# Kernel tuning notes

Measured on AMD Instinct MI355X. Metric: run time of the kernel, lower is better.

Reference implementation:

```python
import jax, jax.numpy as jnp
import numpy as np

B, S, NC, ND, V = 16, 512, 10000, 10000, 128


def _rn(k, shape, scale=0.05):
    return jax.random.normal(k, shape, dtype=jnp.float32) * scale


def setup_inputs() -> dict:
    key = jax.random.key(0)
    ks = jax.random.split(key, 24)
    inp = {
        'c_seq': jax.random.randint(ks[0], (B, S), 0, NC),
        'd_seq': jax.random.randint(ks[1], (B, S), 0, ND),
        'r_seq': jax.random.uniform(ks[2], (B, S), dtype=jnp.float32),
        # embeddings / vectors
        'D1_w': _rn(ks[3], (ND, 1)),
        'D2_w': _rn(ks[4], (ND, V)),
        'v_r': _rn(ks[5], (V,)),
        'v_beta': _rn(ks[6], (V,)),
        # GRU (torch layout: gates ordered r,z,n; W_ih [3V,2V], W_hh [3V,V])
        'W_ih': _rn(ks[7], (3 * V, 2 * V)),
        'W_hh': _rn(ks[8], (3 * V, V)),
        'b_ih': jnp.zeros((3 * V,), jnp.float32),
        'b_hh': jnp.zeros((3 * V,), jnp.float32),
        # linear_1: V -> V -> V -> 1 (weights stored [in, out])
        'm1_W1': _rn(ks[9], (V, V)), 'm1_b1': jnp.zeros((V,), jnp.float32),
        'm1_W2': _rn(ks[10], (V, V)), 'm1_b2': jnp.zeros((V,), jnp.float32),
        'm1_W3': _rn(ks[11], (V, 1)), 'm1_b3': jnp.zeros((1,), jnp.float32),
        # linear_2: 3V -> V -> V -> 1
        'm2_W1': _rn(ks[12], (3 * V, V)), 'm2_b1': jnp.zeros((V,), jnp.float32),
        'm2_W2': _rn(ks[13], (V, V)), 'm2_b2': jnp.zeros((V,), jnp.float32),
        'm2_W3': _rn(ks[14], (V, 1)), 'm2_b3': jnp.zeros((1,), jnp.float32),
    }
    return inp


def _mlp(x, W1, b1, W2, b2, W3, b3):
    h = jax.nn.relu(x @ W1 + b1)
    h = jax.nn.relu(h @ W2 + b2)
    return h @ W3 + b3


def _gru_seq(x, W_ih, W_hh, b_ih, b_hh):
    # x: [B,S,2V] -> h_seq [B,S,V]; torch GRU gate order r,z,n
    xp = x @ W_ih.T + b_ih  # [B,S,3V]

    def step(h, xt):
        hp = h @ W_hh.T + b_hh
        xr, xz, xn = jnp.split(xt, 3, axis=-1)
        hr, hz, hn = jnp.split(hp, 3, axis=-1)
        r = jax.nn.sigmoid(xr + hr)
        z = jax.nn.sigmoid(xz + hz)
        n = jnp.tanh(xn + r * hn)
        h_new = (1.0 - z) * n + z * h
        return h_new, h_new

    h0 = jnp.zeros((x.shape[0], W_hh.shape[1]), x.dtype)
    _, hs = jax.lax.scan(step, h0, jnp.swapaxes(xp, 0, 1))  # [S,B,V]
    return jnp.swapaxes(hs, 0, 1)


def reference(c_seq, d_seq, r_seq, D1_w, D2_w, v_r, v_beta,
              W_ih, W_hh, b_ih, b_hh,
              m1_W1, m1_b1, m1_W2, m1_b2, m1_W3, m1_b3,
              m2_W1, m2_b1, m2_W2, m2_b2, m2_W3, m2_b3):
    v_d_seq = D2_w[d_seq]                     # [B,S,V]
    v_r_seq = r_seq[..., None] * v_r          # [B,S,V]

    h_seq = _gru_seq(jnp.concatenate([v_d_seq, v_r_seq], axis=-1),
                     W_ih, W_hh, b_ih, b_hh)  # [B,S,V]
    alpha_seq = _mlp(h_seq, m1_W1, m1_b1, m1_W2, m1_b2, m1_W3, m1_b3)[..., 0]  # [B,S]

    bidx = jnp.arange(c_seq.shape[0])

    def step(C, ins):
        c_t, vd_t, vr_t = ins                 # [B], [B,V], [B,V]
        beta_prev = C[bidx, c_t]              # gather: [B]
        v_beta_prev = beta_prev[:, None] * v_beta  # [B,V]
        new_c = _mlp(jnp.concatenate([v_beta_prev, vd_t, vr_t], axis=-1),
                     m2_W1, m2_b1, m2_W2, m2_b2, m2_W3, m2_b3)[:, 0]  # [B]
        C = C.at[bidx, c_t].set(new_c)        # scatter
        return C, (C, new_c)

    C0 = jnp.zeros((c_seq.shape[0], NC), jnp.float32)
    _, (C_seq, beta_seq) = jax.lax.scan(
        step, C0,
        (jnp.swapaxes(c_seq, 0, 1), jnp.swapaxes(v_d_seq, 0, 1), jnp.swapaxes(v_r_seq, 0, 1)))
    C_seq = jnp.swapaxes(C_seq, 0, 1)[..., None]   # [B,S,NC,1]
    beta_seq = jnp.swapaxes(beta_seq, 0, 1)        # [B,S]

    gamma_seq = D1_w[d_seq][..., 0]                # [B,S]
    return (alpha_seq, beta_seq, gamma_seq, h_seq, C_seq)
```

## Files before the change

### kernel.cpp

```cpp
#include <hip/hip_runtime.h>

#define Bq   16
#define Sq   512
#define Vq   128
#define NCq  10000

#define OFF_XP     0u
#define OFF_PRE1   3145728u
#define OFF_WTIH   4194304u
#define OFF_W2T    4243456u
#define OFF_WVRIH  4292608u
#define OFF_WVR1   4292992u
#define OFF_WVB    4293120u
#define OFF_PO     4293248u

__global__ __launch_bounds__(256) void k0_prep(
    const int* __restrict__ c_seq, const int* __restrict__ d_seq,
    const float* __restrict__ D1_w,
    const float* __restrict__ W_ih,
    const float* __restrict__ v_r, const float* __restrict__ v_beta,
    const float* __restrict__ m2W1, const float* __restrict__ m2W2,
    float* __restrict__ ws, float* __restrict__ gamma_out)
{
    const int blk = blockIdx.x, tid = threadIdx.x;

    if (blk < 128) {
        float* WTIH = ws + OFF_WTIH;
        int base = blk * 384;
        for (int i = tid; i < 384; i += 256) {
            int e = base + i;
            int k = e / 384, g = e % 384;
            WTIH[e] = W_ih[g * 256 + k];
        }
    } else if (blk == 128) {
        float* WVRIH = ws + OFF_WVRIH;
        float* WVR1  = ws + OFF_WVR1;
        float* WVB   = ws + OFF_WVB;
        for (int g = tid; g < 384; g += 256) {
            float a = 0.f;
            for (int k = 0; k < 128; ++k) a = fmaf(v_r[k], W_ih[g * 256 + 128 + k], a);
            WVRIH[g] = a;
        }
        if (tid < 128) {
            float a = 0.f, b = 0.f;
            for (int k = 0; k < 128; ++k) {
                a = fmaf(v_r[k],    m2W1[(256 + k) * 128 + tid], a);
                b = fmaf(v_beta[k], m2W1[k * 128 + tid],         b);
            }
            WVR1[tid] = a; WVB[tid] = b;
        }
    } else if (blk < 145) {
        const int b = blk - 129;
        __shared__ int cs[Sq];
        for (int i = tid; i < Sq; i += 256) cs[i] = c_seq[b * Sq + i];
        __syncthreads();
        int* PO = (int*)(ws + OFF_PO) + b * Sq;
        for (int t = tid; t < Sq; t += 256) {
            int c = cs[t];
            int po = -1;
            for (int u = t - 1; u >= 0; --u) if (cs[u] == c) { po = u; break; }
            PO[t] = po;
        }
    } else if (blk < 161) {
        const int b = blk - 145;
        for (int s = tid; s < Sq; s += 256)
            gamma_out[b * Sq + s] = D1_w[d_seq[b * Sq + s]];
    } else {
        float* W2T = ws + OFF_W2T;
        for (int e = tid; e < 16384; e += 256) {
            int j = e >> 7, k = e & 127;
            W2T[e] = m2W2[k * 128 + j];
        }
    }
}

__global__ __launch_bounds__(256) void k1_gemm(
    const int* __restrict__ d_seq, const float* __restrict__ D2_w,
    const float* __restrict__ m2W1, float* __restrict__ ws)
{
    __shared__ float As[64 * 128];
    __shared__ float Bs[128 * 64];
    const int blk = blockIdx.x, tid = threadIdx.x;
    const int nc = blk & 7;
    const int m0 = (blk >> 3) * 64;
    const float* WTIH = ws + OFF_WTIH;

    const float4* D2v = (const float4*)D2_w;
    for (int e = tid; e < 2048; e += 256) {
        int r = e >> 5, q = e & 31;
        int d = d_seq[m0 + r];
        *(float4*)&As[r * 128 + 4 * q] = D2v[d * 32 + q];
    }
    for (int e = tid; e < 2048; e += 256) {
        int k = e >> 4, q = e & 15;
        float4 v;
        if (nc < 6) v = *(const float4*)&WTIH[k * 384 + nc * 64 + 4 * q];
        else        v = *(const float4*)&m2W1[(128 + k) * 128 + (nc - 6) * 64 + 4 * q];
        *(float4*)&Bs[k * 64 + 4 * q] = v;
    }
    __syncthreads();

    const int tx = tid & 15, ty = tid >> 4;
    const int c0 = 4 * tx, r0 = 4 * ty;
    float acc[4][4];
#pragma unroll
    for (int i = 0; i < 4; ++i)
#pragma unroll
        for (int j = 0; j < 4; ++j) acc[i][j] = 0.f;

    for (int k = 0; k < 128; ++k) {
        float4 bv = *(const float4*)&Bs[k * 64 + c0];
#pragma unroll
        for (int i = 0; i < 4; ++i) {
            float a = As[(r0 + i) * 128 + k];
            acc[i][0] = fmaf(a, bv.x, acc[i][0]);
            acc[i][1] = fmaf(a, bv.y, acc[i][1]);
            acc[i][2] = fmaf(a, bv.z, acc[i][2]);
            acc[i][3] = fmaf(a, bv.w, acc[i][3]);
        }
    }
    float* XP   = ws + OFF_XP;
    float* PRE1 = ws + OFF_PRE1;
#pragma unroll
    for (int i = 0; i < 4; ++i) {
        int row = m0 + r0 + i;
        float4 v = make_float4(acc[i][0], acc[i][1], acc[i][2], acc[i][3]);
        if (nc < 6) *(float4*)&XP[row * 384 + nc * 64 + c0] = v;
        else        *(float4*)&PRE1[row * 128 + (nc - 6) * 64 + c0] = v;
    }
}

__global__ __launch_bounds__(384, 1) void k2_scan(
    const float* __restrict__ r_seq, const float* __restrict__ W_hh,
    const float* __restrict__ b_ih, const float* __restrict__ b_hh,
    const float* __restrict__ m2b1, const float* __restrict__ m2b2,
    const float* __restrict__ m2W3, const float* __restrict__ m2b3,
    float* __restrict__ ws,
    float* __restrict__ hseq_out, float* __restrict__ beta_out)
{
    __shared__ union {
        struct { float h[128]; float sumr[128]; float sumz[128]; float r[512]; } g;
        struct { float bh[512]; float h1[128]; float red[2]; float r2[512]; int po_[512]; } bt;
    } sm;

    const int blk = blockIdx.x, tid = threadIdx.x;
    const int j = tid & 127;

    if (blk < 16) {
        const int b = blk;
        const int role = tid >> 7;
        const int grow = (role == 0) ? 256 + j : ((role == 1) ? j : 128 + j);

        float4 w4[32];
        {
            const float4* wr = (const float4*)(W_hh + grow * 128);
#pragma unroll
            for (int kk = 0; kk < 32; ++kk) w4[kk] = wr[kk];
        }
        const float wvr = (ws + OFF_WVRIH)[grow];
        const float bih = b_ih[grow];
        const float bhh = b_hh[grow];
        for (int i = tid; i < Sq; i += 384) sm.g.r[i] = r_seq[b * Sq + i];
        if (tid < 128) sm.g.h[tid] = 0.f;
        float h_old = 0.f;
        __syncthreads();

        const float* xpb = ws + OFF_XP + (size_t)b * Sq * 384;
        float xp0 = xpb[grow];
        float xp1 = xpb[384 + grow];
        const float4* h4 = (const float4*)sm.g.h;

        for (int t = 0; t < Sq; ++t) {
            float xp2 = (t < Sq - 2) ? xpb[(t + 2) * 384 + grow] : 0.f;
            float x = fmaf(sm.g.r[t], wvr, xp0 + bih);
            float a0 = 0.f, a1 = 0.f, a2 = 0.f, a3 = 0.f;
#pragma unroll
            for (int kk = 0; kk < 32; ++kk) {
                float4 hv = h4[kk];
                float4 wv = w4[kk];
                a0 = fmaf(wv.x, hv.x, a0);
                a1 = fmaf(wv.y, hv.y, a1);
                a2 = fmaf(wv.z, hv.z, a2);
                a3 = fmaf(wv.w, hv.w, a3);
            }
            float hp = (a0 + a1) + (a2 + a3) + bhh;
            if (role == 1) sm.g.sumr[j] = x + hp;
            else if (role == 2) sm.g.sumz[j] = x + hp;
            __syncthreads();
            if (role == 0) {
                float r = 1.f / (1.f + __expf(-sm.g.sumr[j]));
                float z = 1.f / (1.f + __expf(-sm.g.sumz[j]));
                float npre = fmaf(r, hp, x);
                float ax = fabsf(npre);
                float e2 = __expf(-2.f * ax);
                float n = copysignf((1.f - e2) / (1.f + e2), npre);
                float hnew = (1.f - z) * n + z * h_old;
                h_old = hnew;
                sm.g.h[j] = hnew;
                hseq_out[(size_t)(b * Sq + t) * 128 + j] = hnew;
            }
            __syncthreads();
            xp0 = xp1; xp1 = xp2;
        }
    } else {
        const int b = blk - 16;
        float4 w24[32];
        {
            const float4* wr = (const float4*)(ws + OFF_W2T + j * 128);
#pragma unroll
            for (int kk = 0; kk < 32; ++kk) w24[kk] = wr[kk];
        }
        float wvbj = 0.f, wvr1j = 0.f, b1j = 0.f, b2j = 0.f, w3j = 0.f;
        if (tid < 128) {
            wvbj  = (ws + OFF_WVB)[j];
            wvr1j = (ws + OFF_WVR1)[j];
            b1j = m2b1[j]; b2j = m2b2[j]; w3j = m2W3[j];
        }
        const float b3v = m2b3[0];
        const int* PO = (const int*)(ws + OFF_PO) + b * Sq;
        for (int i = tid; i < Sq; i += 384) {
            sm.bt.r2[i]  = r_seq[b * Sq + i];
            sm.bt.po_[i] = PO[i];
        }
        __syncthreads();

        const float* p1b = ws + OFF_PRE1 + (size_t)b * Sq * 128;
        float p1 = (tid < 128) ? p1b[j] : 0.f;
        const float4* h14 = (const float4*)sm.bt.h1;
        float btap = 0.f;

        for (int t = 0; t < Sq; ++t) {
            float p1n = (tid < 128 && t < Sq - 1) ? p1b[(t + 1) * 128 + j] : 0.f;
            if (tid < 128) {
                int po = sm.bt.po_[t];
                float bp = (po == t - 1) ? btap : ((po >= 0) ? sm.bt.bh[po] : 0.f);
                sm.bt.h1[j] = fmaxf(0.f, fmaf(bp, wvbj, fmaf(sm.bt.r2[t], wvr1j, p1 + b1j)));
            } else if (tid == 128 && t > 0) {
                sm.bt.bh[t - 1] = btap;
            }
            __syncthreads();
            if (tid < 128) {
                float a0 = 0.f, a1 = 0.f, a2 = 0.f, a3 = 0.f;
#pragma unroll
                for (int kk = 0; kk < 32; ++kk) {
                    float4 hv = h14[kk];
                    float4 wv = w24[kk];
                    a0 = fmaf(wv.x, hv.x, a0);
                    a1 = fmaf(wv.y, hv.y, a1);
                    a2 = fmaf(wv.z, hv.z, a2);
                    a3 = fmaf(wv.w, hv.w, a3);
                }
                float h2 = fmaxf(0.f, (a0 + a1) + (a2 + a3) + b2j);
                float part = h2 * w3j;
#pragma unroll
                for (int off = 1; off < 64; off <<= 1) part += __shfl_xor(part, off);
                if ((tid & 63) == 0) sm.bt.red[tid >> 6] = part;
            }
            __syncthreads();
            float bta = sm.bt.red[0] + sm.bt.red[1] + b3v;
            if (tid == 192) beta_out[b * Sq + t] = bta;
            btap = bta;
            p1 = p1n;
        }
    }
}

__global__ __launch_bounds__(256) void k2b_fill(
    const int* __restrict__ c_seq, const float* __restrict__ beta_in,
    float* __restrict__ C_out)
{
    __shared__ int   scs[Sq];
    __shared__ float sbt[Sq];
    const int bid = blockIdx.x, tid = threadIdx.x;
    const int b = bid / 40, rem = bid % 40;
    const int chunk = rem >> 2, q = rem & 3;

    for (int i = tid; i < Sq; i += 256) {
        scs[i] = c_seq[b * Sq + i];
        sbt[i] = beta_in[b * Sq + i];
    }
    __syncthreads();

    const int c0 = chunk * 1024 + tid * 4;
    if (c0 >= NCq) return;

    float cur0 = 0.f, cur1 = 0.f, cur2 = 0.f, cur3 = 0.f;
    const int tlo = q * 128, thi = tlo + 128;
    float* base = C_out + (size_t)b * Sq * NCq + c0;

    for (int t = 0; t < tlo; ++t) {
        int ct = scs[t] - c0; float bv = sbt[t];
        cur0 = (ct == 0) ? bv : cur0;
        cur1 = (ct == 1) ? bv : cur1;
        cur2 = (ct == 2) ? bv : cur2;
        cur3 = (ct == 3) ? bv : cur3;
    }
    for (int t = tlo; t < thi; ++t) {
        int ct = scs[t] - c0; float bv = sbt[t];
        cur0 = (ct == 0) ? bv : cur0;
        cur1 = (ct == 1) ? bv : cur1;
        cur2 = (ct == 2) ? bv : cur2;
        cur3 = (ct == 3) ? bv : cur3;
        *(float4*)(base + (size_t)t * NCq) = make_float4(cur0, cur1, cur2, cur3);
    }
}

__global__ __launch_bounds__(256) void k3_alpha(
    const float* __restrict__ hseq,
    const float* __restrict__ W1, const float* __restrict__ b1,
    const float* __restrict__ W2, const float* __restrict__ b2,
    const float* __restrict__ W3, const float* __restrict__ b3,
    float* __restrict__ alpha_out)
{
    __shared__ float Hs[32 * 128];
    __shared__ float T1[32 * 128];
    __shared__ float red[4][16];
    const int blk = blockIdx.x, tid = threadIdx.x;
    const int row0 = blk * 32;

    for (int e = tid; e < 1024; e += 256) {
        int r = e >> 5, q = e & 31;
        *(float4*)&Hs[r * 128 + 4 * q] =
            *(const float4*)&hseq[(size_t)(row0 + r) * 128 + 4 * q];
    }
    __syncthreads();

    const int j = tid & 127, rh = tid >> 7;
    const float b1j = b1[j], b2j = b2[j], w3j = W3[j];
    float acc[16];
#pragma unroll
    for (int r = 0; r < 16; ++r) acc[r] = b1j;
    for (int k = 0; k < 128; ++k) {
        float w = W1[k * 128 + j];
#pragma unroll
        for (int r = 0; r < 16; ++r)
            acc[r] = fmaf(Hs[(rh * 16 + r) * 128 + k], w, acc[r]);
    }
#pragma unroll
    for (int r = 0; r < 16; ++r) {
        acc[r] = fmaxf(acc[r], 0.f);
        T1[(rh * 16 + r) * 128 + j] = acc[r];
    }
    __syncthreads();
    float acc2[16];
#pragma unroll
    for (int r = 0; r < 16; ++r) acc2[r] = b2j;
    for (int k = 0; k < 128; ++k) {
        float w = W2[k * 128 + j];
#pragma unroll
        for (int r = 0; r < 16; ++r)
            acc2[r] = fmaf(T1[(rh * 16 + r) * 128 + k], w, acc2[r]);
    }
#pragma unroll
    for (int r = 0; r < 16; ++r) {
        float p = fmaxf(acc2[r], 0.f) * w3j;
#pragma unroll
        for (int off = 1; off < 64; off <<= 1) p += __shfl_xor(p, off);
        if ((tid & 63) == 0) red[tid >> 6][r] = p;
    }
    __syncthreads();
    if (tid < 32) {
        int rr = tid & 15, g = tid >> 4;
        alpha_out[row0 + g * 16 + rr] = red[2 * g][rr] + red[2 * g + 1][rr] + b3[0];
    }
}

extern "C" void kernel_launch(void* const* d_in, const int* in_sizes, int n_in,
                              void* d_out, int out_size, void* d_ws, size_t ws_size,
                              hipStream_t stream) {
    const int*   c_seq = (const int*)d_in[0];
    const int*   d_seq = (const int*)d_in[1];
    const float* r_seq = (const float*)d_in[2];
    const float* D1_w  = (const float*)d_in[3];
    const float* D2_w  = (const float*)d_in[4];
    const float* v_r   = (const float*)d_in[5];
    const float* v_b   = (const float*)d_in[6];
    const float* W_ih  = (const float*)d_in[7];
    const float* W_hh  = (const float*)d_in[8];
    const float* b_ih  = (const float*)d_in[9];
    const float* b_hh  = (const float*)d_in[10];
    const float* m1W1  = (const float*)d_in[11];
    const float* m1b1  = (const float*)d_in[12];
    const float* m1W2  = (const float*)d_in[13];
    const float* m1b2  = (const float*)d_in[14];
    const float* m1W3  = (const float*)d_in[15];
    const float* m1b3  = (const float*)d_in[16];
    const float* m2W1  = (const float*)d_in[17];
    const float* m2b1  = (const float*)d_in[18];
    const float* m2W2  = (const float*)d_in[19];
    const float* m2b2  = (const float*)d_in[20];
    const float* m2W3  = (const float*)d_in[21];
    const float* m2b3  = (const float*)d_in[22];

    float* out   = (float*)d_out;
    float* alpha = out;
    float* beta  = out + 8192;
    float* gamma = out + 16384;
    float* hseq  = out + 24576;
    float* Cseq  = out + 1073152;
    float* ws    = (float*)d_ws;

    hipLaunchKernelGGL(k0_prep, dim3(162), dim3(256), 0, stream,
                       c_seq, d_seq, D1_w, W_ih, v_r, v_b, m2W1, m2W2, ws, gamma);
    hipLaunchKernelGGL(k1_gemm, dim3(1024), dim3(256), 0, stream,
                       d_seq, D2_w, m2W1, ws);
    hipLaunchKernelGGL(k2_scan, dim3(32), dim3(384), 0, stream,
                       r_seq, W_hh, b_ih, b_hh, m2b1, m2b2, m2W3, m2b3,
                       ws, hseq, beta);
    hipLaunchKernelGGL(k2b_fill, dim3(640), dim3(256), 0, stream,
                       c_seq, beta, Cseq);
    hipLaunchKernelGGL(k3_alpha, dim3(256), dim3(256), 0, stream,
                       hseq, m1W1, m1b1, m1W2, m1b2, m1W3, m1b3, alpha);
}
```

Measured before the change: 725.3 us.

## Batch GRU and beta scans across sequences using split-bf16 MFMA in two blocks

The two recurrent scans are restructured so that one workgroup processes all 16 batch rows at once. The GRU and the beta-MLP recurrences now use 16x16x32 bf16 MFMA with a hi/lo split (three products) to keep near-fp32 accuracy. The 32 per-batch blocks running scalar dot products are replaced by 2 blocks. Bias and r_seq terms are folded into the GEMM epilogue, and the workspace is relaid out time-major and batch-interleaved to match the MFMA fragments. This trades parallelism across CUs for fewer serial per-step instructions, with some risk from bf16-split precision and from one block doing all the work.

```diff
diff --git a/kernel.cpp b/kernel.cpp
--- a/kernel.cpp
+++ b/kernel.cpp
@@ -5,21 +5,32 @@
 #define Vq   128
 #define NCq  10000
 
+typedef __attribute__((ext_vector_type(8))) short short8v;
+typedef __attribute__((ext_vector_type(4))) float f32x4;
+
 #define OFF_XP     0u
 #define OFF_PRE1   3145728u
 #define OFF_WTIH   4194304u
-#define OFF_W2T    4243456u
-#define OFF_WVRIH  4292608u
-#define OFF_WVR1   4292992u
-#define OFF_WVB    4293120u
-#define OFF_PO     4293248u
+#define OFF_WVRIH  4243456u
+#define OFF_WVR1   4243840u
+#define OFF_WVB    4243968u
+#define OFF_PO     4244096u
+
+__device__ __forceinline__ unsigned short f2bf(float x) {
+    unsigned u = __builtin_bit_cast(unsigned, x);
+    unsigned r = (u + 0x7fffu + ((u >> 16) & 1u)) >> 16;
+    return (unsigned short)r;
+}
+__device__ __forceinline__ float bf2f(unsigned short h) {
+    return __builtin_bit_cast(float, ((unsigned)h) << 16);
+}
 
 __global__ __launch_bounds__(256) void k0_prep(
     const int* __restrict__ c_seq, const int* __restrict__ d_seq,
     const float* __restrict__ D1_w,
     const float* __restrict__ W_ih,
     const float* __restrict__ v_r, const float* __restrict__ v_beta,
-    const float* __restrict__ m2W1, const float* __restrict__ m2W2,
+    const float* __restrict__ m2W1,
     float* __restrict__ ws, float* __restrict__ gamma_out)
 {
     const int blk = blockIdx.x, tid = threadIdx.x;
@@ -54,29 +65,26 @@
         __shared__ int cs[Sq];
         for (int i = tid; i < Sq; i += 256) cs[i] = c_seq[b * Sq + i];
         __syncthreads();
-        int* PO = (int*)(ws + OFF_PO) + b * Sq;
+        int* PO = (int*)(ws + OFF_PO);
         for (int t = tid; t < Sq; t += 256) {
             int c = cs[t];
             int po = -1;
             for (int u = t - 1; u >= 0; --u) if (cs[u] == c) { po = u; break; }
-            PO[t] = po;
-        }
-    } else if (blk < 161) {
+            PO[t * 16 + b] = po;
+        }
+    } else {
         const int b = blk - 145;
         for (int s = tid; s < Sq; s += 256)
             gamma_out[b * Sq + s] = D1_w[d_seq[b * Sq + s]];
-    } else {
-        float* W2T = ws + OFF_W2T;
-        for (int e = tid; e < 16384; e += 256) {
-            int j = e >> 7, k = e & 127;
-            W2T[e] = m2W2[k * 128 + j];
-        }
     }
 }
 
 __global__ __launch_bounds__(256) void k1_gemm(
     const int* __restrict__ d_seq, const float* __restrict__ D2_w,
-    const float* __restrict__ m2W1, float* __restrict__ ws)
+    const float* __restrict__ m2W1,
+    const float* __restrict__ b_ih, const float* __restrict__ b_hh,
+    const float* __restrict__ r_seq, const float* __restrict__ m2b1,
+    float* __restrict__ ws)
 {
     __shared__ float As[64 * 128];
     __shared__ float Bs[128 * 64];
@@ -119,149 +127,294 @@
             acc[i][3] = fmaf(a, bv.w, acc[i][3]);
         }
     }
-    float* XP   = ws + OFF_XP;
-    float* PRE1 = ws + OFF_PRE1;
-#pragma unroll
-    for (int i = 0; i < 4; ++i) {
-        int row = m0 + r0 + i;
-        float4 v = make_float4(acc[i][0], acc[i][1], acc[i][2], acc[i][3]);
-        if (nc < 6) *(float4*)&XP[row * 384 + nc * 64 + c0] = v;
-        else        *(float4*)&PRE1[row * 128 + (nc - 6) * 64 + c0] = v;
-    }
-}
-
-__global__ __launch_bounds__(384, 1) void k2_scan(
-    const float* __restrict__ r_seq, const float* __restrict__ W_hh,
-    const float* __restrict__ b_ih, const float* __restrict__ b_hh,
-    const float* __restrict__ m2b1, const float* __restrict__ m2b2,
+
+    float rsv[4];
+#pragma unroll
+    for (int i = 0; i < 4; ++i) rsv[i] = r_seq[m0 + r0 + i];
+
+    if (nc < 6) {
+        const int grow0 = nc * 64 + c0;
+        float4 bi  = *(const float4*)&b_ih[grow0];
+        float4 wv4 = *(const float4*)&(ws + OFF_WVRIH)[grow0];
+        float4 bh4 = make_float4(0.f, 0.f, 0.f, 0.f);
+        if (nc < 4) bh4 = *(const float4*)&b_hh[grow0];
+        float* XP4 = ws + OFF_XP;
+        const int r4 = grow0 >> 2;
+#pragma unroll
+        for (int i = 0; i < 4; ++i) {
+            int row = m0 + r0 + i;
+            int t = row & 511, bb = row >> 9;
+            float4 v;
+            v.x = acc[i][0] + bi.x + bh4.x + rsv[i] * wv4.x;
+            v.y = acc[i][1] + bi.y + bh4.y + rsv[i] * wv4.y;
+            v.z = acc[i][2] + bi.z + bh4.z + rsv[i] * wv4.z;
+            v.w = acc[i][3] + bi.w + bh4.w + rsv[i] * wv4.w;
+            *(float4*)&XP4[((t * 96 + r4) * 16 + bb) * 4] = v;
+        }
+    } else {
+        const int j0 = (nc - 6) * 64 + c0;
+        float4 b1v = *(const float4*)&m2b1[j0];
+        float4 wr1 = *(const float4*)&(ws + OFF_WVR1)[j0];
+        float* PRE1 = ws + OFF_PRE1;
+#pragma unroll
+        for (int i = 0; i < 4; ++i) {
+            int row = m0 + r0 + i;
+            float4 v;
+            v.x = acc[i][0] + b1v.x + rsv[i] * wr1.x;
+            v.y = acc[i][1] + b1v.y + rsv[i] * wr1.y;
+            v.z = acc[i][2] + b1v.z + rsv[i] * wr1.z;
+            v.w = acc[i][3] + b1v.w + rsv[i] * wr1.w;
+            *(float4*)&PRE1[(size_t)row * 128 + j0] = v;
+        }
+    }
+}
+
+#define PLN 136
+#define PLSZ (16*PLN+8)
+
+__global__ __launch_bounds__(256, 1) void k2_scan(
+    const float* __restrict__ W_hh, const float* __restrict__ b_hh,
+    const float* __restrict__ m2W2, const float* __restrict__ m2b2,
     const float* __restrict__ m2W3, const float* __restrict__ m2b3,
     float* __restrict__ ws,
     float* __restrict__ hseq_out, float* __restrict__ beta_out)
 {
-    __shared__ union {
-        struct { float h[128]; float sumr[128]; float sumz[128]; float r[512]; } g;
-        struct { float bh[512]; float h1[128]; float red[2]; float r2[512]; int po_[512]; } bt;
-    } sm;
-
-    const int blk = blockIdx.x, tid = threadIdx.x;
-    const int j = tid & 127;
-
-    if (blk < 16) {
-        const int b = blk;
-        const int role = tid >> 7;
-        const int grow = (role == 0) ? 256 + j : ((role == 1) ? j : 128 + j);
-
-        float4 w4[32];
+    __shared__ __align__(16) unsigned char smem[74560];
+    const int tid = threadIdx.x;
+    const int l = tid & 63, wv = tid >> 6;
+    const int qq = l >> 4, cb = l & 15;
+
+    if (blockIdx.x == 0) {
+        unsigned short* hHI = (unsigned short*)smem;
+        unsigned short* hLO = (unsigned short*)(smem + 4 * PLSZ);
+        short8v aHI[6][4], aLO[6][4];
+#pragma unroll
+        for (int tau = 0; tau < 6; ++tau) {
+            const int grow = (tau >> 1) * 128 + 32 * wv + (tau & 1) * 16 + cb;
+            const float* wrow = W_hh + grow * 128;
+#pragma unroll
+            for (int kf = 0; kf < 4; ++kf) {
+                short8v hi, lo;
+#pragma unroll
+                for (int e = 0; e < 8; ++e) {
+                    float x = wrow[kf * 32 + qq * 8 + e];
+                    unsigned short hb = f2bf(x);
+                    unsigned short lb = f2bf(x - bf2f(hb));
+                    hi[e] = (short)hb; lo[e] = (short)lb;
+                }
+                aHI[tau][kf] = hi; aLO[tau][kf] = lo;
+            }
+        }
+        float bhhn[2][4];
+#pragma unroll
+        for (int jh = 0; jh < 2; ++jh)
+#pragma unroll
+            for (int i = 0; i < 4; ++i)
+                bhhn[jh][i] = b_hh[256 + 32 * wv + 16 * jh + qq * 4 + i];
+
+        const float* XP4 = ws + OFF_XP;
+        float4 px[6];
+#pragma unroll
+        for (int tau = 0; tau < 6; ++tau) {
+            const int r4 = (tau >> 1) * 32 + 8 * wv + (tau & 1) * 4 + qq;
+            px[tau] = *(const float4*)&XP4[(r4 * 16 + cb) * 4];
+        }
+        float hold[2][4];
+#pragma unroll
+        for (int jh = 0; jh < 2; ++jh)
+#pragma unroll
+            for (int i = 0; i < 4; ++i) hold[jh][i] = 0.f;
+
+        for (int i = tid; i < 2 * PLSZ; i += 256) { hHI[i] = 0; hLO[i] = 0; }
+        __syncthreads();
+
+        for (int t = 0; t < 512; ++t) {
+            const unsigned short* HI = hHI + (t & 1) * PLSZ;
+            const unsigned short* LO = hLO + (t & 1) * PLSZ;
+            unsigned short* HIn = hHI + ((t + 1) & 1) * PLSZ;
+            unsigned short* LOn = hLO + ((t + 1) & 1) * PLSZ;
+
+            f32x4 C[6];
+#pragma unroll
+            for (int tau = 0; tau < 6; ++tau) { C[tau] = (f32x4){0.f, 0.f, 0.f, 0.f}; }
+#pragma unroll
+            for (int kf = 0; kf < 4; ++kf) {
+                short8v Bh = *(const short8v*)(HI + cb * PLN + kf * 32 + qq * 8);
+                short8v Bl = *(const short8v*)(LO + cb * PLN + kf * 32 + qq * 8);
+#pragma unroll
+                for (int tau = 0; tau < 6; ++tau) {
+                    C[tau] = __builtin_amdgcn_mfma_f32_16x16x32_bf16(aHI[tau][kf], Bh, C[tau], 0, 0, 0);
+                    C[tau] = __builtin_amdgcn_mfma_f32_16x16x32_bf16(aHI[tau][kf], Bl, C[tau], 0, 0, 0);
+                    C[tau] = __builtin_amdgcn_mfma_f32_16x16x32_bf16(aLO[tau][kf], Bh, C[tau], 0, 0, 0);
+                }
+            }
+            float4 pxn[6];
+            if (t < 511) {
+#pragma unroll
+                for (int tau = 0; tau < 6; ++tau) {
+                    const int r4 = (tau >> 1) * 32 + 8 * wv + (tau & 1) * 4 + qq;
+                    pxn[tau] = *(const float4*)&XP4[(((t + 1) * 96 + r4) * 16 + cb) * 4];
+                }
+            }
+            float hnew[2][4];
+#pragma unroll
+            for (int jh = 0; jh < 2; ++jh) {
+#pragma unroll
+                for (int i = 0; i < 4; ++i) {
+                    float pr = C[0 + jh][i] + px[0 + jh][i];
+                    float pz = C[2 + jh][i] + px[2 + jh][i];
+                    float r = 1.f / (1.f + __expf(-pr));
+                    float z = 1.f / (1.f + __expf(-pz));
+                    float hn = C[4 + jh][i] + bhhn[jh][i];
+                    float npre = fmaf(r, hn, px[4 + jh][i]);
+                    float ax = fabsf(npre);
+                    float e2 = __expf(-2.f * ax);
+                    float n = copysignf((1.f - e2) / (1.f + e2), npre);
+                    float hv = (1.f - z) * n + z * hold[jh][i];
+                    hold[jh][i] = hv;
+                    hnew[jh][i] = hv;
+                }
+            }
+#pragma unroll
+            for (int jh = 0; jh < 2; ++jh) {
+                *(float4*)&hseq_out[(size_t)(cb * 512 + t) * 128 + 32 * wv + 16 * jh + qq * 4] =
+                    make_float4(hnew[jh][0], hnew[jh][1], hnew[jh][2], hnew[jh][3]);
+                unsigned short hb0 = f2bf(hnew[jh][0]), hb1 = f2bf(hnew[jh][1]);
+                unsigned short hb2 = f2bf(hnew[jh][2]), hb3 = f2bf(hnew[jh][3]);
+                unsigned short lb0 = f2bf(hnew[jh][0] - bf2f(hb0));
+                unsigned short lb1 = f2bf(hnew[jh][1] - bf2f(hb1));
+                unsigned short lb2 = f2bf(hnew[jh][2] - bf2f(hb2));
+                unsigned short lb3 = f2bf(hnew[jh][3] - bf2f(hb3));
+                uint2 hw, lw;
+                hw.x = (unsigned)hb0 | ((unsigned)hb1 << 16);
+                hw.y = (unsigned)hb2 | ((unsigned)hb3 << 16);
+                lw.x = (unsigned)lb0 | ((unsigned)lb1 << 16);
+                lw.y = (unsigned)lb2 | ((unsigned)lb3 << 16);
+                *(uint2*)(HIn + cb * PLN + 32 * wv + 16 * jh + qq * 4) = hw;
+                *(uint2*)(LOn + cb * PLN + 32 * wv + 16 * jh + qq * 4) = lw;
+            }
+#pragma unroll
+            for (int tau = 0; tau < 6; ++tau) px[tau] = pxn[tau];
+            __syncthreads();
+        }
+    } else {
+        float* bhL = (float*)smem;
+        int* poT = (int*)(smem + 32768);
+        unsigned short* h1HI = (unsigned short*)(smem + 65536);
+        unsigned short* h1LO = (unsigned short*)(smem + 69904);
+        float* redL = (float*)(smem + 74272);
+
         {
-            const float4* wr = (const float4*)(W_hh + grow * 128);
-#pragma unroll
-            for (int kk = 0; kk < 32; ++kk) w4[kk] = wr[kk];
-        }
-        const float wvr = (ws + OFF_WVRIH)[grow];
-        const float bih = b_ih[grow];
-        const float bhh = b_hh[grow];
-        for (int i = tid; i < Sq; i += 384) sm.g.r[i] = r_seq[b * Sq + i];
-        if (tid < 128) sm.g.h[tid] = 0.f;
-        float h_old = 0.f;
+            const int* POg = (const int*)(ws + OFF_PO);
+            for (int i = tid; i < 8192; i += 256) poT[i] = POg[i];
+        }
+        short8v aHI[2][4], aLO[2][4];
+#pragma unroll
+        for (int tau = 0; tau < 2; ++tau) {
+            const int j = 32 * wv + 16 * tau + cb;
+#pragma unroll
+            for (int kf = 0; kf < 4; ++kf) {
+                short8v hi, lo;
+#pragma unroll
+                for (int e = 0; e < 8; ++e) {
+                    float x = m2W2[(kf * 32 + qq * 8 + e) * 128 + j];
+                    unsigned short hb = f2bf(x);
+                    unsigned short lb = f2bf(x - bf2f(hb));
+                    hi[e] = (short)hb; lo[e] = (short)lb;
+                }
+                aHI[tau][kf] = hi; aLO[tau][kf] = lo;
+            }
+        }
+        float w3C[2][4], b2C[2][4];
+#pragma unroll
+        for (int tau = 0; tau < 2; ++tau)
+#pragma unroll
+            for (int i = 0; i < 4; ++i) {
+                w3C[tau][i] = m2W3[32 * wv + 16 * tau + qq * 4 + i];
+                b2C[tau][i] = m2b2[32 * wv + 16 * tau + qq * 4 + i];
+            }
+        const float b3v = m2b3[0];
+
+        const int bb2 = tid & 15, j8 = tid >> 4;
+        float wvb[8];
+#pragma unroll
+        for (int e = 0; e < 8; ++e) wvb[e] = (ws + OFF_WVB)[j8 * 8 + e];
+        const float* p1base = ws + OFF_PRE1 + (size_t)(bb2 * 512) * 128 + j8 * 8;
+
+        float4 p1a = *(const float4*)&p1base[0];
+        float4 p1b = *(const float4*)&p1base[4];
         __syncthreads();
 
-        const float* xpb = ws + OFF_XP + (size_t)b * Sq * 384;
-        float xp0 = xpb[grow];
-        float xp1 = xpb[384 + grow];
-        const float4* h4 = (const float4*)sm.g.h;
-
-        for (int t = 0; t < Sq; ++t) {
-            float xp2 = (t < Sq - 2) ? xpb[(t + 2) * 384 + grow] : 0.f;
-            float x = fmaf(sm.g.r[t], wvr, xp0 + bih);
-            float a0 = 0.f, a1 = 0.f, a2 = 0.f, a3 = 0.f;
-#pragma unroll
-            for (int kk = 0; kk < 32; ++kk) {
-                float4 hv = h4[kk];
-                float4 wv = w4[kk];
-                a0 = fmaf(wv.x, hv.x, a0);
-                a1 = fmaf(wv.y, hv.y, a1);
-                a2 = fmaf(wv.z, hv.z, a2);
-                a3 = fmaf(wv.w, hv.w, a3);
-            }
-            float hp = (a0 + a1) + (a2 + a3) + bhh;
-            if (role == 1) sm.g.sumr[j] = x + hp;
-            else if (role == 2) sm.g.sumz[j] = x + hp;
+        for (int t = 0; t < 512; ++t) {
+            int po = poT[t * 16 + bb2];
+            float bp = (po >= 0) ? bhL[bb2 * 512 + po] : 0.f;
+            float hv[8];
+            hv[0] = fmaxf(0.f, fmaf(bp, wvb[0], p1a.x));
+            hv[1] = fmaxf(0.f, fmaf(bp, wvb[1], p1a.y));
+            hv[2] = fmaxf(0.f, fmaf(bp, wvb[2], p1a.z));
+            hv[3] = fmaxf(0.f, fmaf(bp, wvb[3], p1a.w));
+            hv[4] = fmaxf(0.f, fmaf(bp, wvb[4], p1b.x));
+            hv[5] = fmaxf(0.f, fmaf(bp, wvb[5], p1b.y));
+            hv[6] = fmaxf(0.f, fmaf(bp, wvb[6], p1b.z));
+            hv[7] = fmaxf(0.f, fmaf(bp, wvb[7], p1b.w));
+            uint4 hw, lw;
+            {
+                unsigned short h[8], lo[8];
+#pragma unroll
+                for (int e = 0; e < 8; ++e) {
+                    h[e] = f2bf(hv[e]);
+                    lo[e] = f2bf(hv[e] - bf2f(h[e]));
+                }
+                hw.x = (unsigned)h[0] | ((unsigned)h[1] << 16);
+                hw.y = (unsigned)h[2] | ((unsigned)h[3] << 16);
+                hw.z = (unsigned)h[4] | ((unsigned)h[5] << 16);
+                hw.w = (unsigned)h[6] | ((unsigned)h[7] << 16);
+                lw.x = (unsigned)lo[0] | ((unsigned)lo[1] << 16);
+                lw.y = (unsigned)lo[2] | ((unsigned)lo[3] << 16);
+                lw.z = (unsigned)lo[4] | ((unsigned)lo[5] << 16);
+                lw.w = (unsigned)lo[6] | ((unsigned)lo[7] << 16);
+            }
+            *(uint4*)(h1HI + bb2 * PLN + j8 * 8) = hw;
+            *(uint4*)(h1LO + bb2 * PLN + j8 * 8) = lw;
+            float4 p1an, p1bn;
+            if (t < 511) {
+                p1an = *(const float4*)&p1base[(size_t)(t + 1) * 128];
+                p1bn = *(const float4*)&p1base[(size_t)(t + 1) * 128 + 4];
+            }
             __syncthreads();
-            if (role == 0) {
-                float r = 1.f / (1.f + __expf(-sm.g.sumr[j]));
-                float z = 1.f / (1.f + __expf(-sm.g.sumz[j]));
-                float npre = fmaf(r, hp, x);
-                float ax = fabsf(npre);
-                float e2 = __expf(-2.f * ax);
-                float n = copysignf((1.f - e2) / (1.f + e2), npre);
-                float hnew = (1.f - z) * n + z * h_old;
-                h_old = hnew;
-                sm.g.h[j] = hnew;
-                hseq_out[(size_t)(b * Sq + t) * 128 + j] = hnew;
-            }
+
+            f32x4 C[2];
+            C[0] = (f32x4){0.f, 0.f, 0.f, 0.f};
+            C[1] = (f32x4){0.f, 0.f, 0.f, 0.f};
+#pragma unroll
+            for (int kf = 0; kf < 4; ++kf) {
+                short8v Bh = *(const short8v*)(h1HI + cb * PLN + kf * 32 + qq * 8);
+                short8v Bl = *(const short8v*)(h1LO + cb * PLN + kf * 32 + qq * 8);
+#pragma unroll
+                for (int tau = 0; tau < 2; ++tau) {
+                    C[tau] = __builtin_amdgcn_mfma_f32_16x16x32_bf16(aHI[tau][kf], Bh, C[tau], 0, 0, 0);
+                    C[tau] = __builtin_amdgcn_mfma_f32_16x16x32_bf16(aHI[tau][kf], Bl, C[tau], 0, 0, 0);
+                    C[tau] = __builtin_amdgcn_mfma_f32_16x16x32_bf16(aLO[tau][kf], Bh, C[tau], 0, 0, 0);
+                }
+            }
+            float part = 0.f;
+#pragma unroll
+            for (int tau = 0; tau < 2; ++tau)
+#pragma unroll
+                for (int i = 0; i < 4; ++i) {
+                    float h2 = fmaxf(0.f, C[tau][i] + b2C[tau][i]);
+                    part = fmaf(h2, w3C[tau][i], part);
+                }
+            part += __shfl_xor(part, 16);
+            part += __shfl_xor(part, 32);
+            if (l < 16) redL[wv * 16 + l] = part;
             __syncthreads();
-            xp0 = xp1; xp1 = xp2;
-        }
-    } else {
-        const int b = blk - 16;
-        float4 w24[32];
-        {
-            const float4* wr = (const float4*)(ws + OFF_W2T + j * 128);
-#pragma unroll
-            for (int kk = 0; kk < 32; ++kk) w24[kk] = wr[kk];
-        }
-        float wvbj = 0.f, wvr1j = 0.f, b1j = 0.f, b2j = 0.f, w3j = 0.f;
-        if (tid < 128) {
-            wvbj  = (ws + OFF_WVB)[j];
-            wvr1j = (ws + OFF_WVR1)[j];
-            b1j = m2b1[j]; b2j = m2b2[j]; w3j = m2W3[j];
-        }
-        const float b3v = m2b3[0];
-        const int* PO = (const int*)(ws + OFF_PO) + b * Sq;
-        for (int i = tid; i < Sq; i += 384) {
-            sm.bt.r2[i]  = r_seq[b * Sq + i];
-            sm.bt.po_[i] = PO[i];
-        }
-        __syncthreads();
-
-        const float* p1b = ws + OFF_PRE1 + (size_t)b * Sq * 128;
-        float p1 = (tid < 128) ? p1b[j] : 0.f;
-        const float4* h14 = (const float4*)sm.bt.h1;
-        float btap = 0.f;
-
-        for (int t = 0; t < Sq; ++t) {
-            float p1n = (tid < 128 && t < Sq - 1) ? p1b[(t + 1) * 128 + j] : 0.f;
-            if (tid < 128) {
-                int po = sm.bt.po_[t];
-                float bp = (po == t - 1) ? btap : ((po >= 0) ? sm.bt.bh[po] : 0.f);
-                sm.bt.h1[j] = fmaxf(0.f, fmaf(bp, wvbj, fmaf(sm.bt.r2[t], wvr1j, p1 + b1j)));
-            } else if (tid == 128 && t > 0) {
-                sm.bt.bh[t - 1] = btap;
-            }
+            if (tid < 16)
+                bhL[tid * 512 + t] = redL[tid] + redL[16 + tid] + redL[32 + tid] + redL[48 + tid] + b3v;
             __syncthreads();
-            if (tid < 128) {
-                float a0 = 0.f, a1 = 0.f, a2 = 0.f, a3 = 0.f;
-#pragma unroll
-                for (int kk = 0; kk < 32; ++kk) {
-                    float4 hv = h14[kk];
-                    float4 wv = w24[kk];
-                    a0 = fmaf(wv.x, hv.x, a0);
-                    a1 = fmaf(wv.y, hv.y, a1);
-                    a2 = fmaf(wv.z, hv.z, a2);
-                    a3 = fmaf(wv.w, hv.w, a3);
-                }
-                float h2 = fmaxf(0.f, (a0 + a1) + (a2 + a3) + b2j);
-                float part = h2 * w3j;
-#pragma unroll
-                for (int off = 1; off < 64; off <<= 1) part += __shfl_xor(part, off);
-                if ((tid & 63) == 0) sm.bt.red[tid >> 6] = part;
-            }
-            __syncthreads();
-            float bta = sm.bt.red[0] + sm.bt.red[1] + b3v;
-            if (tid == 192) beta_out[b * Sq + t] = bta;
-            btap = bta;
-            p1 = p1n;
-        }
+            p1a = p1an; p1b = p1bn;
+        }
+        for (int i = tid; i < 8192; i += 256) beta_out[i] = bhL[i];
     }
 }
 
@@ -400,13 +553,12 @@
     float* Cseq  = out + 1073152;
     float* ws    = (float*)d_ws;
 
-    hipLaunchKernelGGL(k0_prep, dim3(162), dim3(256), 0, stream,
-                       c_seq, d_seq, D1_w, W_ih, v_r, v_b, m2W1, m2W2, ws, gamma);
+    hipLaunchKernelGGL(k0_prep, dim3(161), dim3(256), 0, stream,
+                       c_seq, d_seq, D1_w, W_ih, v_r, v_b, m2W1, ws, gamma);
     hipLaunchKernelGGL(k1_gemm, dim3(1024), dim3(256), 0, stream,
-                       d_seq, D2_w, m2W1, ws);
-    hipLaunchKernelGGL(k2_scan, dim3(32), dim3(384), 0, stream,
-                       r_seq, W_hh, b_ih, b_hh, m2b1, m2b2, m2W3, m2b3,
-                       ws, hseq, beta);
+                       d_seq, D2_w, m2W1, b_ih, b_hh, r_seq, m2b1, ws);
+    hipLaunchKernelGGL(k2_scan, dim3(2), dim3(256), 0, stream,
+                       W_hh, b_hh, m2W2, m2b2, m2W3, m2b3, ws, hseq, beta);
     hipLaunchKernelGGL(k2b_fill, dim3(640), dim3(256), 0, stream,
                        c_seq, beta, Cseq);
     hipLaunchKernelGGL(k3_alpha, dim3(256), dim3(256), 0, stream,
```

Result: slower. 1.168 ms (+61.0%).
